# Performance work log

Hardware: AMD Instinct MI355X
Metric: run time of the kernel (lower is better)

The kernel has to match this reference:

```python
import jax, jax.numpy as jnp
import numpy as np

BETA = 0.25          # commitment loss weight (init kwarg)
CODEBOOK_SIZE = 2048


def setup_inputs() -> dict:
    key = jax.random.key(0)
    k1, k2 = jax.random.split(key)
    B, L, D = 8, 4096, 256
    z_e = jax.random.normal(k1, (B, L, D), dtype=jnp.float32)
    # xavier_uniform-style init for the codebook
    limit = float(np.sqrt(6.0 / (CODEBOOK_SIZE + D)))
    embed_weight = jax.random.uniform(k2, (CODEBOOK_SIZE, D), dtype=jnp.float32,
                                      minval=-limit, maxval=limit)
    return {"z_e": z_e, "embed_weight": embed_weight}


def reference(z_e, embed_weight):
    # eval-mode forward (no EMA buffer updates)
    B, L, D = z_e.shape
    K = embed_weight.shape[0]
    zf = z_e.reshape(-1, D)                                   # [N, D]
    d2 = (jnp.sum(zf * zf, axis=1, keepdims=True)
          - 2.0 * (zf @ embed_weight.T)
          + jnp.sum(embed_weight * embed_weight, axis=1)[None, :])
    distances = jnp.sqrt(jnp.maximum(d2, 0.0))                # [N, K]
    idx = jnp.argmin(distances, axis=1)                       # [N]
    z_q = embed_weight[idx].reshape(B, L, D)                  # gather

    commitment_loss = BETA * jnp.mean((jax.lax.stop_gradient(z_q) - z_e) ** 2)
    embedding_loss = jnp.mean((jax.lax.stop_gradient(z_e) - z_q) ** 2)

    # avg over one-hot encodings == normalized histogram of idx
    N = zf.shape[0]
    counts = jax.ops.segment_sum(jnp.ones((N,), jnp.float32), idx, num_segments=K)
    avg_probs = counts / N
    perplexity = jnp.exp(-jnp.sum(avg_probs * jnp.log(avg_probs + 1e-10)))
    vq_loss = commitment_loss + embedding_loss - 0.01 * perplexity

    z_q_st = z_e + jax.lax.stop_gradient(z_q - z_e)           # straight-through
    return z_q_st, vq_loss, idx.reshape(B, L)
```

## Files before the change

### kernel.cpp

```cpp
#include <hip/hip_runtime.h>
#include <math.h>

#define DDIM 256
#define NSPLIT 2
#define TILES_PER_SPLIT 32
#define TILE_CODES 32
#define TILE_BYTES 16384
#define ROWS_PER_BLOCK 128

typedef __attribute__((ext_vector_type(8))) short short8v;
typedef __attribute__((ext_vector_type(4))) float float4v;
typedef unsigned int u32;
typedef unsigned short u16;

__device__ __forceinline__ short f2bf(float x) {
    u32 u = __float_as_uint(x);
    u = u + 0x7fffu + ((u >> 16) & 1u);
    return (short)(u >> 16);
}

__device__ __forceinline__ float np_sq_chain(const float* v, int lane) {
    #pragma clang fp contract(off)
    const int half = lane >> 3, j = lane & 7;
    const float* base = v + half * 128 + j;
    float x = base[0];
    float c = x * x;
    #pragma unroll
    for (int m = 1; m < 16; ++m) {
        float y = base[8 * m];
        float s = y * y;
        c = c + s;
    }
    return c;
}

__device__ __forceinline__ float np_combine16(const float* c) {
    #pragma clang fp contract(off)
    float L = ((c[0] + c[1]) + (c[2] + c[3])) + ((c[4] + c[5]) + (c[6] + c[7]));
    float R = ((c[8] + c[9]) + (c[10] + c[11])) + ((c[12] + c[13]) + (c[14] + c[15]));
    return L + R;
}

__device__ __forceinline__ void ins3(float m, int k,
                                     float& v0, float& v1, float& v2,
                                     int& i0, int& i1, int& i2) {
    if (m < v0)      { v2 = v1; i2 = i1; v1 = v0; i1 = i0; v0 = m; i0 = k; }
    else if (m < v1) { v2 = v1; i2 = i1; v1 = m;  i1 = k; }
    else if (m < v2) { v2 = m;  i2 = k; }
}

__global__ void code_norms_np_kernel(const float* __restrict__ e, float* __restrict__ e2,
                                     int* __restrict__ counts) {
    __shared__ float buf[DDIM];
    __shared__ float ch[16];
    int k = blockIdx.x;
    int t = threadIdx.x;
    if (t == 0) counts[k] = 0;
    float4 v = *(const float4*)&e[(size_t)k * DDIM + t * 4];
    *(float4*)&buf[t * 4] = v;
    __syncthreads();
    if (t < 16) ch[t] = np_sq_chain(buf, t);
    __syncthreads();
    if (t == 0) e2[k] = np_combine16(ch);
}

__global__ void convert_permute_e_kernel(const float* __restrict__ e, char* __restrict__ ebf_p) {
    int id = blockIdx.x * 256 + threadIdx.x;
    int k = id >> 5, d8 = id & 31;
    const float* s = &e[(size_t)k * DDIM + d8 * 8];
    float4 f0 = *(const float4*)s;
    float4 f1 = *(const float4*)(s + 4);
    short8v v;
    v[0] = f2bf(f0.x); v[1] = f2bf(f0.y); v[2] = f2bf(f0.z); v[3] = f2bf(f0.w);
    v[4] = f2bf(f1.x); v[5] = f2bf(f1.y); v[6] = f2bf(f1.z); v[7] = f2bf(f1.w);
    *(short8v*)(ebf_p + ((size_t)(k >> 5) << 14) + d8 * 512 + (k & 31) * 16) = v;
}

__global__ __launch_bounds__(512, 1)
void vq_cand_kernel(const float* __restrict__ z, const char* __restrict__ ebf_p,
                    const float* __restrict__ e2, float* __restrict__ cand_v,
                    u16* __restrict__ cand_i, int N) {
    __shared__ float e2s[1024];
    const int t    = threadIdx.x;
    const int w    = t >> 6;
    const int lane = t & 63;
    const int quad = lane >> 4;
    const int l15  = lane & 15;
    const int s    = blockIdx.y;
    const int rw   = blockIdx.x * ROWS_PER_BLOCK + w * 16;

    e2s[t]       = e2[s * 1024 + t];
    e2s[t + 512] = e2[s * 1024 + 512 + t];

    short8v zf0, zf1, zf2, zf3, zf4, zf5, zf6, zf7;
    {
        const float* zr = &z[(size_t)(rw + l15) * DDIM];
#define LOADZ(I, DST)                                                        \
        {                                                                    \
            int d0 = (I) * 32 + quad * 8;                                    \
            float4 f0 = *(const float4*)&zr[d0];                             \
            float4 f1 = *(const float4*)&zr[d0 + 4];                         \
            short8v v;                                                       \
            v[0] = f2bf(f0.x); v[1] = f2bf(f0.y);                            \
            v[2] = f2bf(f0.z); v[3] = f2bf(f0.w);                            \
            v[4] = f2bf(f1.x); v[5] = f2bf(f1.y);                            \
            v[6] = f2bf(f1.z); v[7] = f2bf(f1.w);                            \
            DST = v;                                                         \
        }
        LOADZ(0, zf0) LOADZ(1, zf1) LOADZ(2, zf2) LOADZ(3, zf3)
        LOADZ(4, zf4) LOADZ(5, zf5) LOADZ(6, zf6) LOADZ(7, zf7)
#undef LOADZ
    }

    __syncthreads();

    float v0 = 3.4e38f, v1 = 3.4e38f, v2 = 3.4e38f;
    int   i0 = 0x7fff,  i1 = 0x7fff,  i2 = 0x7fff;

    const char* sbase = ebf_p + (size_t)s * TILES_PER_SPLIT * TILE_BYTES
                      + quad * 512 + l15 * 16;

    #pragma unroll 1
    for (int tt = 0; tt < TILES_PER_SPLIT; ++tt) {
        const char* tg = sbase + (size_t)tt * TILE_BYTES;

        float4v acc0 = (float4v)0.0f, acc1 = (float4v)0.0f;

#define STEP(KK, ZF)                                                         \
        {                                                                    \
            short8v a0 = *(const short8v*)(tg + (KK) * 2048);                \
            short8v a1 = *(const short8v*)(tg + (KK) * 2048 + 256);          \
            acc0 = __builtin_amdgcn_mfma_f32_16x16x32_bf16(a0, ZF, acc0, 0, 0, 0); \
            acc1 = __builtin_amdgcn_mfma_f32_16x16x32_bf16(a1, ZF, acc1, 0, 0, 0); \
        }
        STEP(0, zf0) STEP(1, zf1) STEP(2, zf2) STEP(3, zf3)
        STEP(4, zf4) STEP(5, zf5) STEP(6, zf6) STEP(7, zf7)
#undef STEP

        const int kloc  = tt * TILE_CODES;
        const int kbase = s * 1024 + kloc;
        float4 e2a = *(const float4*)&e2s[kloc + quad * 4];
        float4 e2b = *(const float4*)&e2s[kloc + 16 + quad * 4];
        float m;
        m = fmaf(-2.0f, acc0[0], e2a.x); ins3(m, kbase + quad * 4 + 0,      v0, v1, v2, i0, i1, i2);
        m = fmaf(-2.0f, acc1[0], e2b.x); ins3(m, kbase + 16 + quad * 4 + 0, v0, v1, v2, i0, i1, i2);
        m = fmaf(-2.0f, acc0[1], e2a.y); ins3(m, kbase + quad * 4 + 1,      v0, v1, v2, i0, i1, i2);
        m = fmaf(-2.0f, acc1[1], e2b.y); ins3(m, kbase + 16 + quad * 4 + 1, v0, v1, v2, i0, i1, i2);
        m = fmaf(-2.0f, acc0[2], e2a.z); ins3(m, kbase + quad * 4 + 2,      v0, v1, v2, i0, i1, i2);
        m = fmaf(-2.0f, acc1[2], e2b.z); ins3(m, kbase + 16 + quad * 4 + 2, v0, v1, v2, i0, i1, i2);
        m = fmaf(-2.0f, acc0[3], e2a.w); ins3(m, kbase + quad * 4 + 3,      v0, v1, v2, i0, i1, i2);
        m = fmaf(-2.0f, acc1[3], e2b.w); ins3(m, kbase + 16 + quad * 4 + 3, v0, v1, v2, i0, i1, i2);
    }

    {
        float bm0 = 3.4e38f, bm1 = 3.4e38f, bm2 = 3.4e38f;
        int   bk0 = 0x7fff,  bk1 = 0x7fff,  bk2 = 0x7fff;
        #pragma unroll
        for (int q = 0; q < 4; ++q) {
            int src = l15 + q * 16;
            float m0 = __shfl(v0, src); int k0 = __shfl(i0, src);
            float m1 = __shfl(v1, src); int k1 = __shfl(i1, src);
            float m2 = __shfl(v2, src); int k2 = __shfl(i2, src);
            ins3(m0, k0, bm0, bm1, bm2, bk0, bk1, bk2);
            ins3(m1, k1, bm0, bm1, bm2, bk0, bk1, bk2);
            ins3(m2, k2, bm0, bm1, bm2, bk0, bk1, bk2);
        }
        if (quad == 0) {
            size_t base = ((size_t)s * N + (rw + l15)) * 3;
            cand_v[base]     = bm0;  cand_i[base]     = (u16)bk0;
            cand_v[base + 1] = bm1;  cand_i[base + 1] = (u16)bk1;
            cand_v[base + 2] = bm2;  cand_i[base + 2] = (u16)bk2;
        }
    }
}

__global__ void refine_fused_kernel(const float* __restrict__ z, const float* __restrict__ e,
                                    const float* __restrict__ e2np,
                                    const float* __restrict__ cand_v,
                                    const u16* __restrict__ cand_i,
                                    int* __restrict__ counts, float* __restrict__ partials,
                                    float* __restrict__ out_zq, float* __restrict__ out_idx,
                                    int N) {
    __shared__ float buf[4][DDIM];
    __shared__ float ch[4][16];
    __shared__ float wsum[4];
    const int w = threadIdx.x >> 6;
    const int t = threadIdx.x & 63;
    const int n = blockIdx.x * 4 + w;

    float4 zv = *(const float4*)&z[(size_t)n * DDIM + t * 4];
    *(float4*)&buf[w][t * 4] = zv;
    __syncthreads();
    if (t < 16) ch[w][t] = np_sq_chain(buf[w], t);
    __syncthreads();

    float bv[6]; int bi[6];
    #pragma unroll
    for (int c = 0; c < 6; ++c) { bv[c] = 3.4e38f; bi[c] = 0x7fffffff; }
    #pragma unroll
    for (int c = 0; c < 6; ++c) {
        int sp = c / 3, j = c - sp * 3;
        size_t off = ((size_t)sp * N + n) * 3 + j;
        float v  = cand_v[off];
        int   id = (int)cand_i[off];
        #pragma unroll
        for (int x = 0; x < 6; ++x) {
            if (v < bv[x] || (v == bv[x] && id < bi[x])) {
                for (int d = 5; d > x; --d) { bv[d] = bv[d - 1]; bi[d] = bi[d - 1]; }
                bv[x] = v; bi[x] = id;
                break;
            }
        }
    }

    float dotf[6];
    #pragma unroll
    for (int c = 0; c < 6; ++c) {
        int k = bi[c];
        float4 ev = *(const float4*)&e[(size_t)k * DDIM + t * 4];
        double p = (double)zv.x * (double)ev.x + (double)zv.y * (double)ev.y
                 + (double)zv.z * (double)ev.z + (double)zv.w * (double)ev.w;
        #pragma unroll
        for (int o = 32; o > 0; o >>= 1) p += __shfl_down(p, o);
        dotf[c] = (float)p;
    }

    int bk = 0;
    if (t == 0) {
        #pragma clang fp contract(off)
        float sx = np_combine16(ch[w]);
        float bd = 3.4e38f;
        bk = 0x7fffffff;
        #pragma unroll
        for (int c = 0; c < 6; ++c) {
            float twod = 2.0f * dotf[c];
            float t1 = sx - twod;
            float d2v = t1 + e2np[bi[c]];
            d2v = fmaxf(d2v, 0.0f);
            float d = sqrtf(d2v);
            if (d < bd || (d == bd && bi[c] < bk)) { bd = d; bk = bi[c]; }
        }
    }
    int wk = __shfl(bk, 0);

    float4 ev = *(const float4*)&e[(size_t)wk * DDIM + t * 4];
    *(float4*)&out_zq[(size_t)n * DDIM + t * 4] = ev;
    float dx = zv.x - ev.x, dy = zv.y - ev.y, dz = zv.z - ev.z, dw = zv.w - ev.w;
    float sq = dx * dx + dy * dy + dz * dz + dw * dw;
    #pragma unroll
    for (int o = 32; o > 0; o >>= 1) sq += __shfl_down(sq, o);
    if (t == 0) {
        wsum[w] = sq;
        atomicAdd(&counts[wk], 1);
        out_idx[n] = (float)wk;
    }
    __syncthreads();
    if (threadIdx.x == 0)
        partials[blockIdx.x] = wsum[0] + wsum[1] + wsum[2] + wsum[3];
}

__global__ void finalize_kernel(const int* __restrict__ counts, const float* __restrict__ partials,
                                float* __restrict__ out_loss, int K, int NB,
                                float invN, float invND) {
    int t = threadIdx.x;
    double ent = 0.0, sq = 0.0;
    for (int k = t; k < K; k += 256) {
        float p = (float)counts[k] * invN;
        ent += (double)(p * logf(p + 1e-10f));
    }
    for (int i = t; i < NB; i += 256) sq += (double)partials[i];
    #pragma unroll
    for (int o = 32; o > 0; o >>= 1) {
        ent += __shfl_down(ent, o);
        sq  += __shfl_down(sq, o);
    }
    __shared__ double e4[4], s4[4];
    if ((t & 63) == 0) { e4[t >> 6] = ent; s4[t >> 6] = sq; }
    __syncthreads();
    if (t == 0) {
        double esum = e4[0] + e4[1] + e4[2] + e4[3];
        double ssum = s4[0] + s4[1] + s4[2] + s4[3];
        float perp = expf((float)(-esum));
        float mean = (float)ssum * invND;
        out_loss[0] = 1.25f * mean - 0.01f * perp;
    }
}

extern "C" void kernel_launch(void* const* d_in, const int* in_sizes, int n_in,
                              void* d_out, int out_size, void* d_ws, size_t ws_size,
                              hipStream_t stream) {
    const float* z = (const float*)d_in[0];
    const float* e = (const float*)d_in[1];
    const int N = in_sizes[0] / DDIM;
    const int K = in_sizes[1] / DDIM;

    float* out      = (float*)d_out;
    float* out_zq   = out;
    float* out_loss = out + (size_t)N * DDIM;
    float* out_idx  = out_loss + 1;

    int*   counts   = (int*)d_ws;
    float* e2np     = (float*)((char*)d_ws + 8192);
    float* partials = (float*)((char*)d_ws + 16384);
    float* cand_v   = (float*)((char*)d_ws + 49152);
    u16*   cand_i   = (u16*)((char*)d_ws + 835584);
    char*  ebf_p    = (char*)d_ws + 1228800;

    code_norms_np_kernel<<<K, 64, 0, stream>>>(e, e2np, counts);
    convert_permute_e_kernel<<<K * 32 / 256, 256, 0, stream>>>(e, ebf_p);
    vq_cand_kernel<<<dim3(N / ROWS_PER_BLOCK, NSPLIT), 512, 0, stream>>>(z, ebf_p, e2np,
                                                                         cand_v, cand_i, N);
    refine_fused_kernel<<<N / 4, 256, 0, stream>>>(z, e, e2np, cand_v, cand_i,
                                                   counts, partials, out_zq, out_idx, N);
    finalize_kernel<<<1, 256, 0, stream>>>(counts, partials, out_loss, K, N / 4,
                                           1.0f / (float)N, 1.0f / (float)(N * DDIM));
}
```

Measured before the change: 402.8 us.

## Process two row groups per wave and split codebook four ways

Each wave now keeps two 16-row z fragments in registers and runs both through the same codebook A-fragment loads, so each global load of codebook data feeds twice the MFMA work. The codebook is split into 4 slices instead of 2, with 256 rows per block, and launch bounds now allow 2 blocks per CU. The refine kernel merges 12 candidates instead of 6, and the workspace offsets grow to fit the larger candidate buffers. This raises register pressure and the candidate-merge cost in exchange for less load traffic per MFMA and more blocks in flight.

```diff
diff --git a/kernel.cpp b/kernel.cpp
--- a/kernel.cpp
+++ b/kernel.cpp
@@ -2,11 +2,11 @@
 #include <math.h>
 
 #define DDIM 256
-#define NSPLIT 2
-#define TILES_PER_SPLIT 32
+#define NSPLIT 4
+#define TILES_PER_SPLIT 16
 #define TILE_CODES 32
 #define TILE_BYTES 16384
-#define ROWS_PER_BLOCK 128
+#define ROWS_PER_BLOCK 256
 
 typedef __attribute__((ext_vector_type(8))) short short8v;
 typedef __attribute__((ext_vector_type(4))) float float4v;
@@ -76,30 +76,31 @@
     *(short8v*)(ebf_p + ((size_t)(k >> 5) << 14) + d8 * 512 + (k & 31) * 16) = v;
 }
 
-__global__ __launch_bounds__(512, 1)
+__global__ __launch_bounds__(512, 2)
 void vq_cand_kernel(const float* __restrict__ z, const char* __restrict__ ebf_p,
                     const float* __restrict__ e2, float* __restrict__ cand_v,
                     u16* __restrict__ cand_i, int N) {
-    __shared__ float e2s[1024];
+    __shared__ float e2s[512];
     const int t    = threadIdx.x;
     const int w    = t >> 6;
     const int lane = t & 63;
     const int quad = lane >> 4;
     const int l15  = lane & 15;
     const int s    = blockIdx.y;
-    const int rw   = blockIdx.x * ROWS_PER_BLOCK + w * 16;
-
-    e2s[t]       = e2[s * 1024 + t];
-    e2s[t + 512] = e2[s * 1024 + 512 + t];
+    const int rw   = blockIdx.x * ROWS_PER_BLOCK + w * 32;
+
+    e2s[t] = e2[s * 512 + t];
 
     short8v zf0, zf1, zf2, zf3, zf4, zf5, zf6, zf7;
+    short8v zg0, zg1, zg2, zg3, zg4, zg5, zg6, zg7;
     {
-        const float* zr = &z[(size_t)(rw + l15) * DDIM];
-#define LOADZ(I, DST)                                                        \
+        const float* zrA = &z[(size_t)(rw + l15) * DDIM];
+        const float* zrB = &z[(size_t)(rw + 16 + l15) * DDIM];
+#define LOADZ(SRC, I, DST)                                                   \
         {                                                                    \
             int d0 = (I) * 32 + quad * 8;                                    \
-            float4 f0 = *(const float4*)&zr[d0];                             \
-            float4 f1 = *(const float4*)&zr[d0 + 4];                         \
+            float4 f0 = *(const float4*)&SRC[d0];                            \
+            float4 f1 = *(const float4*)&SRC[d0 + 4];                        \
             short8v v;                                                       \
             v[0] = f2bf(f0.x); v[1] = f2bf(f0.y);                            \
             v[2] = f2bf(f0.z); v[3] = f2bf(f0.w);                            \
@@ -107,15 +108,19 @@
             v[6] = f2bf(f1.z); v[7] = f2bf(f1.w);                            \
             DST = v;                                                         \
         }
-        LOADZ(0, zf0) LOADZ(1, zf1) LOADZ(2, zf2) LOADZ(3, zf3)
-        LOADZ(4, zf4) LOADZ(5, zf5) LOADZ(6, zf6) LOADZ(7, zf7)
+        LOADZ(zrA, 0, zf0) LOADZ(zrA, 1, zf1) LOADZ(zrA, 2, zf2) LOADZ(zrA, 3, zf3)
+        LOADZ(zrA, 4, zf4) LOADZ(zrA, 5, zf5) LOADZ(zrA, 6, zf6) LOADZ(zrA, 7, zf7)
+        LOADZ(zrB, 0, zg0) LOADZ(zrB, 1, zg1) LOADZ(zrB, 2, zg2) LOADZ(zrB, 3, zg3)
+        LOADZ(zrB, 4, zg4) LOADZ(zrB, 5, zg5) LOADZ(zrB, 6, zg6) LOADZ(zrB, 7, zg7)
 #undef LOADZ
     }
 
     __syncthreads();
 
-    float v0 = 3.4e38f, v1 = 3.4e38f, v2 = 3.4e38f;
-    int   i0 = 0x7fff,  i1 = 0x7fff,  i2 = 0x7fff;
+    float va0 = 3.4e38f, va1 = 3.4e38f, va2 = 3.4e38f;
+    int   ia0 = 0x7fff,  ia1 = 0x7fff,  ia2 = 0x7fff;
+    float vb0 = 3.4e38f, vb1 = 3.4e38f, vb2 = 3.4e38f;
+    int   ib0 = 0x7fff,  ib1 = 0x7fff,  ib2 = 0x7fff;
 
     const char* sbase = ebf_p + (size_t)s * TILES_PER_SPLIT * TILE_BYTES
                       + quad * 512 + l15 * 16;
@@ -124,49 +129,73 @@
     for (int tt = 0; tt < TILES_PER_SPLIT; ++tt) {
         const char* tg = sbase + (size_t)tt * TILE_BYTES;
 
-        float4v acc0 = (float4v)0.0f, acc1 = (float4v)0.0f;
-
-#define STEP(KK, ZF)                                                         \
+        float4v acc00 = (float4v)0.0f, acc01 = (float4v)0.0f;
+        float4v acc10 = (float4v)0.0f, acc11 = (float4v)0.0f;
+
+#define STEP(KK, ZF, ZG)                                                     \
         {                                                                    \
             short8v a0 = *(const short8v*)(tg + (KK) * 2048);                \
             short8v a1 = *(const short8v*)(tg + (KK) * 2048 + 256);          \
-            acc0 = __builtin_amdgcn_mfma_f32_16x16x32_bf16(a0, ZF, acc0, 0, 0, 0); \
-            acc1 = __builtin_amdgcn_mfma_f32_16x16x32_bf16(a1, ZF, acc1, 0, 0, 0); \
-        }
-        STEP(0, zf0) STEP(1, zf1) STEP(2, zf2) STEP(3, zf3)
-        STEP(4, zf4) STEP(5, zf5) STEP(6, zf6) STEP(7, zf7)
+            acc00 = __builtin_amdgcn_mfma_f32_16x16x32_bf16(a0, ZF, acc00, 0, 0, 0); \
+            acc01 = __builtin_amdgcn_mfma_f32_16x16x32_bf16(a1, ZF, acc01, 0, 0, 0); \
+            acc10 = __builtin_amdgcn_mfma_f32_16x16x32_bf16(a0, ZG, acc10, 0, 0, 0); \
+            acc11 = __builtin_amdgcn_mfma_f32_16x16x32_bf16(a1, ZG, acc11, 0, 0, 0); \
+        }
+        STEP(0, zf0, zg0) STEP(1, zf1, zg1) STEP(2, zf2, zg2) STEP(3, zf3, zg3)
+        STEP(4, zf4, zg4) STEP(5, zf5, zg5) STEP(6, zf6, zg6) STEP(7, zf7, zg7)
 #undef STEP
 
         const int kloc  = tt * TILE_CODES;
-        const int kbase = s * 1024 + kloc;
+        const int kbase = s * 512 + kloc;
         float4 e2a = *(const float4*)&e2s[kloc + quad * 4];
         float4 e2b = *(const float4*)&e2s[kloc + 16 + quad * 4];
         float m;
-        m = fmaf(-2.0f, acc0[0], e2a.x); ins3(m, kbase + quad * 4 + 0,      v0, v1, v2, i0, i1, i2);
-        m = fmaf(-2.0f, acc1[0], e2b.x); ins3(m, kbase + 16 + quad * 4 + 0, v0, v1, v2, i0, i1, i2);
-        m = fmaf(-2.0f, acc0[1], e2a.y); ins3(m, kbase + quad * 4 + 1,      v0, v1, v2, i0, i1, i2);
-        m = fmaf(-2.0f, acc1[1], e2b.y); ins3(m, kbase + 16 + quad * 4 + 1, v0, v1, v2, i0, i1, i2);
-        m = fmaf(-2.0f, acc0[2], e2a.z); ins3(m, kbase + quad * 4 + 2,      v0, v1, v2, i0, i1, i2);
-        m = fmaf(-2.0f, acc1[2], e2b.z); ins3(m, kbase + 16 + quad * 4 + 2, v0, v1, v2, i0, i1, i2);
-        m = fmaf(-2.0f, acc0[3], e2a.w); ins3(m, kbase + quad * 4 + 3,      v0, v1, v2, i0, i1, i2);
-        m = fmaf(-2.0f, acc1[3], e2b.w); ins3(m, kbase + 16 + quad * 4 + 3, v0, v1, v2, i0, i1, i2);
+        m = fmaf(-2.0f, acc00[0], e2a.x); ins3(m, kbase + quad * 4 + 0,      va0, va1, va2, ia0, ia1, ia2);
+        m = fmaf(-2.0f, acc01[0], e2b.x); ins3(m, kbase + 16 + quad * 4 + 0, va0, va1, va2, ia0, ia1, ia2);
+        m = fmaf(-2.0f, acc10[0], e2a.x); ins3(m, kbase + quad * 4 + 0,      vb0, vb1, vb2, ib0, ib1, ib2);
+        m = fmaf(-2.0f, acc11[0], e2b.x); ins3(m, kbase + 16 + quad * 4 + 0, vb0, vb1, vb2, ib0, ib1, ib2);
+        m = fmaf(-2.0f, acc00[1], e2a.y); ins3(m, kbase + quad * 4 + 1,      va0, va1, va2, ia0, ia1, ia2);
+        m = fmaf(-2.0f, acc01[1], e2b.y); ins3(m, kbase + 16 + quad * 4 + 1, va0, va1, va2, ia0, ia1, ia2);
+        m = fmaf(-2.0f, acc10[1], e2a.y); ins3(m, kbase + quad * 4 + 1,      vb0, vb1, vb2, ib0, ib1, ib2);
+        m = fmaf(-2.0f, acc11[1], e2b.y); ins3(m, kbase + 16 + quad * 4 + 1, vb0, vb1, vb2, ib0, ib1, ib2);
+        m = fmaf(-2.0f, acc00[2], e2a.z); ins3(m, kbase + quad * 4 + 2,      va0, va1, va2, ia0, ia1, ia2);
+        m = fmaf(-2.0f, acc01[2], e2b.z); ins3(m, kbase + 16 + quad * 4 + 2, va0, va1, va2, ia0, ia1, ia2);
+        m = fmaf(-2.0f, acc10[2], e2a.z); ins3(m, kbase + quad * 4 + 2,      vb0, vb1, vb2, ib0, ib1, ib2);
+        m = fmaf(-2.0f, acc11[2], e2b.z); ins3(m, kbase + 16 + quad * 4 + 2, vb0, vb1, vb2, ib0, ib1, ib2);
+        m = fmaf(-2.0f, acc00[3], e2a.w); ins3(m, kbase + quad * 4 + 3,      va0, va1, va2, ia0, ia1, ia2);
+        m = fmaf(-2.0f, acc01[3], e2b.w); ins3(m, kbase + 16 + quad * 4 + 3, va0, va1, va2, ia0, ia1, ia2);
+        m = fmaf(-2.0f, acc10[3], e2a.w); ins3(m, kbase + quad * 4 + 3,      vb0, vb1, vb2, ib0, ib1, ib2);
+        m = fmaf(-2.0f, acc11[3], e2b.w); ins3(m, kbase + 16 + quad * 4 + 3, vb0, vb1, vb2, ib0, ib1, ib2);
     }
 
     {
+        float am0 = 3.4e38f, am1 = 3.4e38f, am2 = 3.4e38f;
+        int   ak0 = 0x7fff,  ak1 = 0x7fff,  ak2 = 0x7fff;
         float bm0 = 3.4e38f, bm1 = 3.4e38f, bm2 = 3.4e38f;
         int   bk0 = 0x7fff,  bk1 = 0x7fff,  bk2 = 0x7fff;
         #pragma unroll
         for (int q = 0; q < 4; ++q) {
             int src = l15 + q * 16;
-            float m0 = __shfl(v0, src); int k0 = __shfl(i0, src);
-            float m1 = __shfl(v1, src); int k1 = __shfl(i1, src);
-            float m2 = __shfl(v2, src); int k2 = __shfl(i2, src);
+            float m0 = __shfl(va0, src); int k0 = __shfl(ia0, src);
+            float m1 = __shfl(va1, src); int k1 = __shfl(ia1, src);
+            float m2 = __shfl(va2, src); int k2 = __shfl(ia2, src);
+            ins3(m0, k0, am0, am1, am2, ak0, ak1, ak2);
+            ins3(m1, k1, am0, am1, am2, ak0, ak1, ak2);
+            ins3(m2, k2, am0, am1, am2, ak0, ak1, ak2);
+            m0 = __shfl(vb0, src); k0 = __shfl(ib0, src);
+            m1 = __shfl(vb1, src); k1 = __shfl(ib1, src);
+            m2 = __shfl(vb2, src); k2 = __shfl(ib2, src);
             ins3(m0, k0, bm0, bm1, bm2, bk0, bk1, bk2);
             ins3(m1, k1, bm0, bm1, bm2, bk0, bk1, bk2);
             ins3(m2, k2, bm0, bm1, bm2, bk0, bk1, bk2);
         }
         if (quad == 0) {
             size_t base = ((size_t)s * N + (rw + l15)) * 3;
+            cand_v[base]     = am0;  cand_i[base]     = (u16)ak0;
+            cand_v[base + 1] = am1;  cand_i[base + 1] = (u16)ak1;
+            cand_v[base + 2] = am2;  cand_i[base + 2] = (u16)ak2;
+        } else if (quad == 1) {
+            size_t base = ((size_t)s * N + (rw + 16 + l15)) * 3;
             cand_v[base]     = bm0;  cand_i[base]     = (u16)bk0;
             cand_v[base + 1] = bm1;  cand_i[base + 1] = (u16)bk1;
             cand_v[base + 2] = bm2;  cand_i[base + 2] = (u16)bk2;
@@ -198,7 +227,7 @@
     #pragma unroll
     for (int c = 0; c < 6; ++c) { bv[c] = 3.4e38f; bi[c] = 0x7fffffff; }
     #pragma unroll
-    for (int c = 0; c < 6; ++c) {
+    for (int c = 0; c < 12; ++c) {
         int sp = c / 3, j = c - sp * 3;
         size_t off = ((size_t)sp * N + n) * 3 + j;
         float v  = cand_v[off];
@@ -303,8 +332,8 @@
     float* e2np     = (float*)((char*)d_ws + 8192);
     float* partials = (float*)((char*)d_ws + 16384);
     float* cand_v   = (float*)((char*)d_ws + 49152);
-    u16*   cand_i   = (u16*)((char*)d_ws + 835584);
-    char*  ebf_p    = (char*)d_ws + 1228800;
+    u16*   cand_i   = (u16*)((char*)d_ws + 1622016);
+    char*  ebf_p    = (char*)d_ws + 2408448;
 
     code_norms_np_kernel<<<K, 64, 0, stream>>>(e, e2np, counts);
     convert_permute_e_kernel<<<K * 32 / 256, 256, 0, stream>>>(e, ebf_p);
```

Measured after the change: 547.7 us. 36.0% more time.
